# Optimization experiments

Measured on AMD Instinct MI355X. Metric: run time of the kernel, lower is better.

The kernel has to match this reference:

```python
import jax, jax.numpy as jnp
import numpy as np
from jax import lax

NPOINT = 1024
FG_NSAMPLE = 512
TOPK = 2048
NSAMPLE = 32
RADIUS = 0.3
BN_EPS = 1e-5


def masked_fps(xyz, mask, n):
    """Farthest point sampling restricted to points where mask is True.
    xyz: [B,N,3] (grad-stopped), mask: [B,N] bool. Returns int32 [B,n] indices.
    Equivalent to running FPS on the masked subset starting at its first point."""
    xyz = lax.stop_gradient(xyz)

    def one(x, m):
        mind0 = jnp.where(m, jnp.float32(1e10), jnp.float32(-1.0))

        def body(i, carry):
            mind, idxs = carry
            sel = jnp.argmax(mind).astype(jnp.int32)
            d = jnp.sum((x - x[sel]) ** 2, axis=-1)
            mind = jnp.where(m, jnp.minimum(mind, d), jnp.float32(-1.0))
            return mind, idxs.at[i].set(sel)

        _, idxs = lax.fori_loop(0, n, body, (mind0, jnp.zeros((n,), jnp.int32)))
        return idxs

    return jax.vmap(one)(xyz, mask)


def ball_query(xyz, new_xyz, radius, nsample):
    """xyz: [B,N,3], new_xyz: [B,S,3] -> int32 [B,S,nsample] of first neighbors
    within radius (padded with the first found index, as in pointnet2 CUDA)."""
    x = lax.stop_gradient(xyz)
    q = lax.stop_gradient(new_xyz)
    d2 = jnp.sum((q[:, :, None, :] - x[:, None, :, :]) ** 2, axis=-1)  # [B,S,N]
    N = x.shape[1]
    ar = jnp.arange(N, dtype=jnp.float32)
    key = jnp.where(d2 <= radius * radius, ar, jnp.float32(N))
    neg_top, _ = lax.top_k(-key, nsample)  # smallest nsample indices
    idx = (-neg_top).astype(jnp.int32)
    first = idx[..., :1]
    idx = jnp.where(idx >= N, first, idx)
    return jnp.clip(idx, 0, N - 1)


def conv_bn_relu_2d(x, W, g, b):
    # x: [B,C,S,ns], W: [O,C]; 1x1 conv (no bias) + training-mode BN + ReLU
    y = jnp.einsum('oc,bcsn->bosn', W, x)
    mu = y.mean((0, 2, 3), keepdims=True)
    var = y.var((0, 2, 3), keepdims=True)
    y = (y - mu) * lax.rsqrt(var + BN_EPS) * g[None, :, None, None] + b[None, :, None, None]
    return jax.nn.relu(y)


def conv_bn_relu_1d(x, W, g, b):
    # x: [B,C,N]
    y = jnp.einsum('oc,bcn->bon', W, x)
    mu = y.mean((0, 2), keepdims=True)
    var = y.var((0, 2), keepdims=True)
    y = (y - mu) * lax.rsqrt(var + BN_EPS) * g[None, :, None] + b[None, :, None]
    return jax.nn.relu(y)


def batch_gather_points(x, idx):
    # x: [B,N,3], idx: [B,...] -> [B,...,3]
    return jax.vmap(lambda a, i: a[i])(x, idx)


def batch_gather_feats(f, idx):
    # f: [B,C,N], idx: [B,S,ns] -> [B,C,S,ns]
    return jax.vmap(lambda a, i: a[:, i])(f, idx)


def setup_inputs() -> dict:
    key = jax.random.key(0)
    ks = jax.random.split(key, 16)
    B, N, C = 4, 16384, 128
    s = 0.05
    return {
        'xyz': jax.random.uniform(ks[0], (B, N, 3), dtype=jnp.float32),
        'features': jax.random.normal(ks[1], (B, C, N), dtype=jnp.float32),
        # grouped shared MLP: (3+C)->128->128->256
        'w1': jax.random.normal(ks[2], (128, 131), dtype=jnp.float32) * s,
        'g1': jnp.ones((128,), jnp.float32), 'b1': jnp.zeros((128,), jnp.float32),
        'w2': jax.random.normal(ks[3], (128, 128), dtype=jnp.float32) * s,
        'g2': jnp.ones((128,), jnp.float32), 'b2': jnp.zeros((128,), jnp.float32),
        'w3': jax.random.normal(ks[4], (256, 128), dtype=jnp.float32) * s,
        'g3': jnp.ones((256,), jnp.float32), 'b3': jnp.zeros((256,), jnp.float32),
        # fbs mask MLP: C->64->2 (last layer plain conv with bias)
        'fw1': jax.random.normal(ks[5], (64, 128), dtype=jnp.float32) * s,
        'fg1': jnp.ones((64,), jnp.float32), 'fb1': jnp.zeros((64,), jnp.float32),
        'fw2': jax.random.normal(ks[6], (2, 64), dtype=jnp.float32) * s,
        'fbias2': jnp.zeros((2,), jnp.float32),
    }


def reference(xyz, features, w1, g1, b1, w2, g2, b2, w3, g3, b3, fw1, fg1, fb1, fw2, fbias2):
    B, N, _ = xyz.shape
    # --- FBS: foreground/background scoring ---
    h = conv_bn_relu_1d(features, fw1, fg1, fb1)                 # [B,64,N]
    mask_scores = jnp.einsum('oc,bcn->bon', fw2, h) + fbias2[None, :, None]  # [B,2,N]
    soft = jax.nn.softmax(mask_scores, axis=1)
    margin = soft[:, 1, :] - soft[:, 0, :]                        # [B,N]
    _, top_idx = lax.top_k(margin, TOPK)
    fg_mask = jnp.zeros((B, N), bool).at[jnp.arange(B)[:, None], top_idx].set(True)
    # --- mask-restricted FPS on foreground and background ---
    fg_idx = masked_fps(xyz, fg_mask, FG_NSAMPLE)                 # [B,512]
    bg_idx = masked_fps(xyz, ~fg_mask, NPOINT - FG_NSAMPLE)       # [B,512]
    indices = jnp.concatenate([fg_idx, bg_idx], axis=1)          # [B,npoint]
    new_xyz = batch_gather_points(xyz, indices)                   # [B,npoint,3]
    # --- ball query + grouping ---
    idx = ball_query(xyz, new_xyz, RADIUS, NSAMPLE)               # [B,S,ns]
    grouped_xyz = batch_gather_points(xyz, idx)                   # [B,S,ns,3]
    grouped_xyz = grouped_xyz - new_xyz[:, :, None, :]
    grouped_xyz = jnp.transpose(grouped_xyz, (0, 3, 1, 2))        # [B,3,S,ns]
    grouped_feats = batch_gather_feats(features, idx)             # [B,C,S,ns]
    x = jnp.concatenate([grouped_xyz, grouped_feats], axis=1)     # [B,3+C,S,ns]
    # --- shared MLP + max pool over neighbors ---
    x = conv_bn_relu_2d(x, w1, g1, b1)
    x = conv_bn_relu_2d(x, w2, g2, b2)
    x = conv_bn_relu_2d(x, w3, g3, b3)
    new_features = jnp.max(x, axis=-1)                            # [B,256,S]
    return new_xyz, new_features, indices, mask_scores
```

## Files before the change

kernel.cpp:

```cpp
#include <hip/hip_runtime.h>

#define BB 4
#define NPT 16384
#define CIN 128
#define SS 1024
#define NS 32
#define PP 131072
#define TOPKK 2048

typedef unsigned short u16;
typedef unsigned int u32;
typedef unsigned long long u64;
typedef float v2 __attribute__((ext_vector_type(2)));
typedef short bf16x8 __attribute__((ext_vector_type(8)));
typedef float f32x4 __attribute__((ext_vector_type(4)));

__device__ __forceinline__ float bf2f(u32 v){ return __uint_as_float(v << 16); }
__device__ __forceinline__ u16 f2bf(float f){
  u32 u = __float_as_uint(f);
  u32 r = (u + 0x7FFFu + ((u >> 16) & 1u)) >> 16;
  return (u16)r;
}
__device__ __forceinline__ u32 keyOf(float m){
  u32 u = __float_as_uint(m);
  return (u & 0x80000000u) ? ~u : (u | 0x80000000u);
}

__device__ __forceinline__ float row_max16(float v){
  #define STEP(CTRL) { int o_ = __builtin_amdgcn_update_dpp(0, __float_as_int(v), CTRL, 0xf, 0xf, true); \
                       v = fmaxf(v, __int_as_float(o_)); }
  STEP(0x111) STEP(0x112) STEP(0x114) STEP(0x118)
  #undef STEP
  return v;
}

#define OFF_NEWXYZ 0ull
#define OFF_MARGIN 49152ull
#define OFF_FGMASK 311296ull
#define OFF_IDXNB  573440ull
#define OFF_MSTAT  1097728ull
#define OFF_SSA    1098240ull
#define OFF_WT0    1104384ull
#define OFF_W1B    1137152ull
#define OFF_W2B    1178112ull
#define OFF_W3B    1210880ull
#define OFF_MPART  1407488ull
#define OFF_CPART  2456064ull
#define OFF_REGB   10844672ull
#define OFF_REGA   44399104ull
#define WS_NEED    86342144ull

__global__ void k_prep(const float* __restrict__ w1, const float* __restrict__ w2,
                       const float* __restrict__ w3, const float* __restrict__ fw1,
                       float* __restrict__ wt0, u16* __restrict__ w1b, u16* __restrict__ w2b,
                       u16* __restrict__ w3b){
  int gt = blockIdx.x*blockDim.x + threadIdx.x;
  int gs = gridDim.x*blockDim.x;
  for (int i = gt; i < 128*64;  i += gs){ int k=i>>6, m=i&63;  wt0[i] = fw1[m*128+k]; }
  for (int i = gt; i < 128*160; i += gs){ int m=i/160, k=i-m*160; w1b[i] = (k<131)? f2bf(w1[m*131+k]) : (u16)0; }
  for (int i = gt; i < 128*128; i += gs){ w2b[i] = f2bf(w2[i]); }
  for (int i = gt; i < 256*128; i += gs){ w3b[i] = f2bf(w3[i]); }
}

__global__ __launch_bounds__(256) void k_prepT(const float* __restrict__ feat, u16* __restrict__ featT2){
  __shared__ u16 tile[128][66];
  int b = blockIdx.y; int n0 = blockIdx.x * 64;
  int t = threadIdx.x;
  #pragma unroll
  for (int it = 0; it < 32; it++){
    int idx = it*256 + t; int c = idx >> 6, nn = idx & 63;
    tile[c][nn] = f2bf(feat[((size_t)b*CIN + c)*NPT + n0 + nn]);
  }
  __syncthreads();
  for (int it = 0; it < 40; it++){
    int idx = it*256 + t; int nn = idx / 160; int c = idx - nn*160;
    u16 v = (c >= 3 && c < 131) ? tile[c-3][nn] : (u16)0;
    featT2[((size_t)(b*NPT + n0 + nn))*160 + c] = v;
  }
}

__global__ __launch_bounds__(256) void k_gemm_mask(const float* __restrict__ Wt,
                                                   const float* __restrict__ feat,
                                                   float* __restrict__ y0,
                                                   double* __restrict__ mpart){
  __shared__ float As[32][64];
  __shared__ float Bs[32][64];
  int t = threadIdx.x, tx = t & 15, ty = t >> 4;
  int p0 = blockIdx.x * 64; int b = blockIdx.z;
  const float* X = feat + (size_t)b * CIN * NPT;
  float acc[4][4] = {};
  int e = t * 8, ka = e >> 6, ca = e & 63;
  for (int kc = 0; kc < 4; kc++){
    const float* wr = Wt + (size_t)(kc*32 + ka) * 64 + ca;
    float4 w0 = *(const float4*)wr;
    float4 w1v = *(const float4*)(wr + 4);
    const float* br = X + (size_t)(kc*32 + ka) * NPT + p0 + ca;
    float4 b0 = *(const float4*)br;
    float4 b1 = *(const float4*)(br + 4);
    __syncthreads();
    *(float4*)&As[ka][ca] = w0; *(float4*)&As[ka][ca+4] = w1v;
    *(float4*)&Bs[ka][ca] = b0; *(float4*)&Bs[ka][ca+4] = b1;
    __syncthreads();
    #pragma unroll
    for (int k = 0; k < 32; k++){
      float4 a = *(float4*)&As[k][ty*4];
      float4 bq = *(float4*)&Bs[k][tx*4];
      float av[4] = {a.x,a.y,a.z,a.w}; float bw[4] = {bq.x,bq.y,bq.z,bq.w};
      #pragma unroll
      for (int i = 0; i < 4; i++)
        #pragma unroll
        for (int j = 0; j < 4; j++) acc[i][j] = fmaf(av[i], bw[j], acc[i][j]);
    }
  }
  #pragma unroll
  for (int i = 0; i < 4; i++){
    int m = ty*4 + i;
    float4 v = make_float4(acc[i][0], acc[i][1], acc[i][2], acc[i][3]);
    *(float4*)(y0 + ((size_t)(b*64 + m)) * NPT + p0 + tx*4) = v;
  }
  __syncthreads();
  float* red = (float*)As;
  #pragma unroll
  for (int i = 0; i < 4; i++){
    float s = 0.f, q = 0.f;
    #pragma unroll
    for (int j = 0; j < 4; j++){ s += acc[i][j]; q += acc[i][j]*acc[i][j]; }
    red[((ty*4+i)*16 + tx)*2] = s; red[((ty*4+i)*16 + tx)*2 + 1] = q;
  }
  __syncthreads();
  if (t < 64){
    double s = 0.0, q = 0.0;
    for (int x = 0; x < 16; x++){ s += red[(t*16+x)*2]; q += red[(t*16+x)*2+1]; }
    int slot = b*256 + blockIdx.x;
    mpart[((size_t)t*1024 + slot)*2] = s;
    mpart[((size_t)t*1024 + slot)*2 + 1] = q;
  }
}

__global__ void k_mask_stats(const double* __restrict__ mpart, float* __restrict__ mstat){
  int t = threadIdx.x;
  double s = 0.0, q = 0.0;
  for (int i = 0; i < 1024; i++){ s += mpart[((size_t)t*1024 + i)*2]; q += mpart[((size_t)t*1024 + i)*2+1]; }
  double cnt = 65536.0;
  double mu = s/cnt; double var = q/cnt - mu*mu;
  mstat[t*2] = (float)mu; mstat[t*2+1] = 1.0f / sqrtf((float)var + 1e-5f);
}

__global__ __launch_bounds__(256) void k_scores(const float* __restrict__ y0, const float* __restrict__ mstat,
                                                const float* __restrict__ fg1, const float* __restrict__ fb1,
                                                const float* __restrict__ fw2, const float* __restrict__ fbias2,
                                                float* __restrict__ margin, float* __restrict__ out3){
  __shared__ float smu[64], srs[64], sg[64], sb[64], sw[128];
  int t = threadIdx.x; int b = blockIdx.y; int n = blockIdx.x*256 + t;
  if (t < 64){ smu[t] = mstat[t*2]; srs[t] = mstat[t*2+1]; sg[t] = fg1[t]; sb[t] = fb1[t]; }
  if (t < 128) sw[t] = fw2[t];
  __syncthreads();
  float a0 = 0.f, a1 = 0.f;
  const float* yb = y0 + (size_t)b*64*NPT + n;
  for (int o = 0; o < 64; o++){
    float y = yb[(size_t)o * NPT];
    float h = __fmul_rn(__fmul_rn(__fsub_rn(y, smu[o]), srs[o]), sg[o]);
    h = __fadd_rn(h, sb[o]);
    h = fmaxf(h, 0.f);
    a0 = fmaf(sw[o], h, a0);
    a1 = fmaf(sw[64+o], h, a1);
  }
  float s0 = __fadd_rn(a0, fbias2[0]);
  float s1 = __fadd_rn(a1, fbias2[1]);
  out3[(size_t)(b*2)*NPT + n] = s0;
  out3[(size_t)(b*2+1)*NPT + n] = s1;
  float m = fmaxf(s0, s1);
  float e0 = expf(__fsub_rn(s0, m));
  float e1 = expf(__fsub_rn(s1, m));
  float den = __fadd_rn(e0, e1);
  margin[b*NPT + n] = __fsub_rn(__fdiv_rn(e1, den), __fdiv_rn(e0, den));
}

__global__ __launch_bounds__(1024) void k_topk(const float* __restrict__ margin, u32* __restrict__ fgmask){
  int t = threadIdx.x; int b = blockIdx.x;
  int lane = t & 63, wv = t >> 6;
  const float* mg = margin + b*NPT; u32* fm = fgmask + b*NPT;
  __shared__ int hist[256];
  __shared__ int swt[2][16];
  __shared__ u32 s_bin; __shared__ int s_need;
  int need = TOPKK; u32 prefix = 0, kmask = 0;
  for (int r = 0; r < 4; r++){
    int shift = 24 - 8*r;
    if (t < 256) hist[t] = 0;
    __syncthreads();
    for (int j = 0; j < 16; j++){
      u32 key = keyOf(mg[j*1024 + t]);
      if ((key & kmask) == prefix) atomicAdd(&hist[(key >> shift) & 255], 1);
    }
    __syncthreads();
    if (t == 0){
      int cum = 0;
      for (int bin = 255; bin >= 0; bin--){
        int c = hist[bin];
        if (cum + c >= need){ s_bin = (u32)bin; s_need = need - cum; break; }
        cum += c;
      }
    }
    __syncthreads();
    prefix |= s_bin << shift; kmask |= 255u << shift; need = s_need;
    __syncthreads();
  }
  u32 T = prefix;
  int run = 0;
  for (int j = 0; j < 16; j++){
    int n = j*1024 + t;
    u32 key = keyOf(mg[n]);
    int eq = (key == T) ? 1 : 0;
    int gt = (key > T) ? 1 : 0;
    u64 bal = __ballot(eq != 0);
    int lexcl = __popcll(bal & ((1ull << lane) - 1ull));
    if (lane == 0) swt[j & 1][wv] = __popcll(bal);
    __syncthreads();
    int base = 0, tot = 0;
    #pragma unroll
    for (int w = 0; w < 16; w++){
      int c = swt[j & 1][w];
      tot += c;
      if (w < wv) base += c;
    }
    int flag = gt | (eq & ((run + base + lexcl) < need ? 1 : 0));
    fm[n] = (u32)flag;
    run += tot;
  }
}

__global__ __launch_bounds__(1024) void k_compact(const float* __restrict__ xyz, const u32* __restrict__ fgmask,
                                                  float* __restrict__ cx, float* __restrict__ cy,
                                                  float* __restrict__ cz, int* __restrict__ cg){
  int blk = blockIdx.x; int b = blk >> 1; int which = blk & 1;
  const float* xb = xyz + (size_t)b * NPT * 3;
  const u32* mb = fgmask + b*NPT;
  int t = threadIdx.x;
  __shared__ int sc[1024];
  u32 mloc = 0; int cnt = 0;
  int p0 = t*16;
  #pragma unroll
  for (int j = 0; j < 16; j++){
    u32 m = mb[p0+j];
    bool inc = which ? (m == 0u) : (m != 0u);
    mloc |= (inc ? 1u : 0u) << j; cnt += inc ? 1 : 0;
  }
  sc[t] = cnt; __syncthreads();
  for (int off = 1; off < 1024; off <<= 1){
    int v = (t >= off) ? sc[t-off] : 0;
    __syncthreads();
    sc[t] += v;
    __syncthreads();
  }
  int pos = sc[t] - cnt;
  int base = b*16384 + (which ? 2048 : 0);
  for (int j = 0; j < 16; j++){
    if ((mloc >> j) & 1u){
      int p = p0 + j;
      cx[base+pos] = xb[p*3]; cy[base+pos] = xb[p*3+1]; cz[base+pos] = xb[p*3+2];
      cg[base+pos] = p; pos++;
    }
  }
}

template<int NV>
__device__ __forceinline__ void fps_run(const float* __restrict__ cx, const float* __restrict__ cy,
                                        const float* __restrict__ cz, const int* __restrict__ cg,
                                        int b, int which,
                                        float* __restrict__ newxyz, float* __restrict__ out0,
                                        float* __restrict__ out2){
  #pragma clang fp contract(off)
  int t = threadIdx.x;
  __shared__ u64 slots[2][8];
  if (t < 16) ((u64*)slots)[t] = 0ull;
  v2 px[NV], py[NV], pz[NV], mind[NV];
  #pragma unroll
  for (int r = 0; r < NV; r++){
    int p0 = 1024*r + t, p1 = 1024*r + 512 + t;
    px[r].x = cx[p0]; px[r].y = cx[p1];
    py[r].x = cy[p0]; py[r].y = cy[p1];
    pz[r].x = cz[p0]; pz[r].y = cz[p1];
    mind[r].x = 1e10f; mind[r].y = 1e10f;
  }
  __syncthreads();
  float bv = 1e10f; int bi = t;
  for (int it = 0; it < 512; it++){
    u64 key = ((u64)(it+1) << 46) | ((u64)keyOf(bv) << 14) | (u64)(16383 - bi);
    atomicMax((unsigned long long*)&slots[it & 1][t & 7], (unsigned long long)key);
    __syncthreads();
    u64 k0 = slots[it & 1][0];
    #pragma unroll
    for (int i = 1; i < 8; i++){ u64 ki = slots[it & 1][i]; if (ki > k0) k0 = ki; }
    int sel = 16383 - (int)(k0 & 0x3FFFu);
    float xs = cx[sel], ys = cy[sel], zs = cz[sel];
    if (t == 0){
      int s = which*512 + it;
      out2[b*1024 + s] = (float)cg[sel];
      newxyz[(b*1024 + s)*3]   = xs;
      newxyz[(b*1024 + s)*3+1] = ys;
      newxyz[(b*1024 + s)*3+2] = zs;
      out0[(b*1024 + s)*3]   = xs;
      out0[(b*1024 + s)*3+1] = ys;
      out0[(b*1024 + s)*3+2] = zs;
    }
    v2 xs2; xs2.x = xs; xs2.y = xs;
    v2 ys2; ys2.x = ys; ys2.y = ys;
    v2 zs2; zs2.x = zs; zs2.y = zs;
    bv = -1.0f; bi = 16383;
    #pragma unroll
    for (int r = 0; r < NV; r++){
      v2 dx = px[r] - xs2;
      v2 dy = py[r] - ys2;
      v2 dz = pz[r] - zs2;
      v2 qx = dx * dx;
      v2 qy = dy * dy;
      v2 qz = dz * dz;
      v2 s1 = qx + qy;
      v2 d  = s1 + qz;
      float m0 = fminf(mind[r].x, d.x);
      float m1 = fminf(mind[r].y, d.y);
      mind[r].x = m0; mind[r].y = m1;
      if (m0 > bv){ bv = m0; bi = 1024*r + t; }
      if (m1 > bv){ bv = m1; bi = 1024*r + 512 + t; }
    }
  }
}

__global__ __launch_bounds__(512) void k_fps(const float* __restrict__ cx, const float* __restrict__ cy,
                                             const float* __restrict__ cz, const int* __restrict__ cg,
                                             float* __restrict__ newxyz, float* __restrict__ out0,
                                             float* __restrict__ out2){
  int b = blockIdx.x >> 1; int which = blockIdx.x & 1;
  int base = b*16384 + (which ? 2048 : 0);
  if (which) fps_run<14>(cx+base, cy+base, cz+base, cg+base, b, 1, newxyz, out0, out2);
  else       fps_run<2 >(cx+base, cy+base, cz+base, cg+base, b, 0, newxyz, out0, out2);
}

__global__ __launch_bounds__(256) void k_ball(const float* __restrict__ xyz, const float* __restrict__ newxyz,
                                              int* __restrict__ idxnb){
  int t = threadIdx.x; int lane = t & 63;
  int qid = blockIdx.x*4 + (t >> 6);
  int b = qid >> 10;
  const float* xb = xyz + (size_t)b * NPT * 3;
  float qx = newxyz[qid*3], qy = newxyz[qid*3+1], qz = newxyz[qid*3+2];
  int found = 0, first = -1;
  for (int base = 0; base < NPT; base += 64){
    int p = base + lane;
    float x = xb[p*3], y = xb[p*3+1], z = xb[p*3+2];
    float dx = __fsub_rn(qx, x), dy = __fsub_rn(qy, y), dz = __fsub_rn(qz, z);
    float d2 = __fadd_rn(__fadd_rn(__fmul_rn(dx,dx), __fmul_rn(dy,dy)), __fmul_rn(dz,dz));
    bool w = d2 <= 0.09f;
    u64 m = __ballot(w);
    if (first < 0 && m) first = base + __ffsll((unsigned long long)m) - 1;
    if (w){
      int pos = found + __popcll(m & ((1ull << lane) - 1ull));
      if (pos < NS) idxnb[(size_t)qid*NS + pos] = p;
    }
    found += __popcll(m);
    if (found >= NS) break;
  }
  if (first < 0) first = 0;
  if (lane < NS && lane >= found) idxnb[(size_t)qid*NS + lane] = first;
}

__global__ __launch_bounds__(256) void k_buildX(const float* __restrict__ xyz, const float* __restrict__ newxyz,
                                                const int* __restrict__ idxnb, const u16* __restrict__ featT2,
                                                u16* __restrict__ Xb2){
  int pos = blockIdx.x*256 + threadIdx.x;
  int b = pos >> 15; int r = pos & 32767; int s = r >> 5;
  int gi = idxnb[pos] & (NPT - 1);
  const float* xp = xyz + ((size_t)b*NPT + gi) * 3;
  const float* qp = newxyz + ((size_t)(b << 10) + s) * 3;
  u16 d0 = f2bf(__fsub_rn(xp[0], qp[0]));
  u16 d1 = f2bf(__fsub_rn(xp[1], qp[1]));
  u16 d2 = f2bf(__fsub_rn(xp[2], qp[2]));
  const uint4* row = (const uint4*)(featT2 + (size_t)(b*NPT + gi) * 160);
  #pragma unroll
  for (int kg = 0; kg < 20; kg++){
    uint4 u = row[kg];
    if (kg == 0){
      u.x = (u32)d0 | ((u32)d1 << 16);
      u.y = (u.y & 0xFFFF0000u) | (u32)d2;
    }
    *(uint4*)(Xb2 + ((size_t)kg*PP + pos)*8) = u;
  }
}

template<int NKS, int STORE>
__global__ __launch_bounds__(256) void k_mfma(const u16* __restrict__ Wb, int Kpad,
                                              const u16* __restrict__ Xp,
                                              u16* __restrict__ Yp, double* __restrict__ cpart){
  __shared__ float sred[4][16][16][2];
  int t = threadIdx.x;
  int w = t >> 6, lane = t & 63;
  int q = lane >> 4, c = lane & 15;
  int p0 = blockIdx.x * 64, m0 = blockIdx.y * 64;
  int m_w = m0 + w*16;
  f32x4 acc[4] = {{0.f,0.f,0.f,0.f},{0.f,0.f,0.f,0.f},{0.f,0.f,0.f,0.f},{0.f,0.f,0.f,0.f}};
  const u16* arow = Wb + (size_t)(m_w + c) * Kpad + q*8;
  #pragma unroll
  for (int ks = 0; ks < NKS; ks++){
    bf16x8 afrag = *(const bf16x8*)(arow + ks*32);
    #pragma unroll
    for (int pp = 0; pp < 4; pp++){
      int p = p0 + pp*16 + c;
      bf16x8 bfrag = *(const bf16x8*)(Xp + (((size_t)(ks*4 + q) * PP) + p) * 8);
      acc[pp] = __builtin_amdgcn_mfma_f32_16x16x32_bf16(afrag, bfrag, acc[pp], 0, 0, 0);
    }
  }
  #pragma unroll
  for (int reg = 0; reg < 4; reg++){
    float s = 0.f, sq = 0.f;
    #pragma unroll
    for (int pp = 0; pp < 4; pp++){ float v = acc[pp][reg]; s += v; sq += v*v; }
    sred[w][q*4+reg][c][0] = s; sred[w][q*4+reg][c][1] = sq;
  }
  if (STORE){
    int kgm = (m_w + q*4) >> 3;
    int j0 = (m_w + q*4) & 7;
    #pragma unroll
    for (int pp = 0; pp < 4; pp++){
      int p = p0 + pp*16 + c;
      ushort4 pk;
      pk.x = f2bf(acc[pp][0]); pk.y = f2bf(acc[pp][1]); pk.z = f2bf(acc[pp][2]); pk.w = f2bf(acc[pp][3]);
      *(ushort4*)(Yp + (((size_t)kgm * PP) + p) * 8 + j0) = pk;
    }
  }
  __syncthreads();
  if (t < 64){
    int ww = t >> 4, ml = t & 15;
    double s = 0.0, qq = 0.0;
    for (int cc = 0; cc < 16; cc++){ s += sred[ww][ml][cc][0]; qq += sred[ww][ml][cc][1]; }
    cpart[((size_t)(m0 + t) * 2048 + blockIdx.x)*2] = s;
    cpart[((size_t)(m0 + t) * 2048 + blockIdx.x)*2 + 1] = qq;
  }
}

__global__ __launch_bounds__(256) void k_mfma_pool(const u16* __restrict__ Wb,
                                                   const u16* __restrict__ Xp,
                                                   const float2* __restrict__ ss2,
                                                   float* __restrict__ out1){
  int t = threadIdx.x;
  int w = t >> 6, lane = t & 63;
  int q = lane >> 4, c = lane & 15;
  int p0 = blockIdx.x * 64, m0 = blockIdx.y * 64;
  int m_w = m0 + w*16;
  f32x4 acc[4] = {{0.f,0.f,0.f,0.f},{0.f,0.f,0.f,0.f},{0.f,0.f,0.f,0.f},{0.f,0.f,0.f,0.f}};
  const u16* arow = Wb + (size_t)(m_w + c) * 128 + q*8;
  #pragma unroll
  for (int ks = 0; ks < 4; ks++){
    bf16x8 afrag = *(const bf16x8*)(arow + ks*32);
    #pragma unroll
    for (int pp = 0; pp < 4; pp++){
      int p = p0 + pp*16 + c;
      bf16x8 bfrag = *(const bf16x8*)(Xp + (((size_t)(ks*4 + q) * PP) + p) * 8);
      acc[pp] = __builtin_amdgcn_mfma_f32_16x16x32_bf16(afrag, bfrag, acc[pp], 0, 0, 0);
    }
  }
  int qid0 = blockIdx.x*2;
  #pragma unroll
  for (int reg = 0; reg < 4; reg++){
    int m = m_w + q*4 + reg;
    float2 af = ss2[m];
    float x0 = fmaxf(0.f, fmaf(acc[0][reg], af.x, af.y));
    float x1 = fmaxf(0.f, fmaf(acc[1][reg], af.x, af.y));
    float x2 = fmaxf(0.f, fmaf(acc[2][reg], af.x, af.y));
    float x3 = fmaxf(0.f, fmaf(acc[3][reg], af.x, af.y));
    float v0 = row_max16(fmaxf(x0, x1));
    float v1 = row_max16(fmaxf(x2, x3));
    if (c == 15){
      int qa = qid0, qb = qid0 + 1;
      out1[((size_t)(qa >> 10) << 18) + (size_t)m*1024 + (qa & 1023)] = v0;
      out1[((size_t)(qb >> 10) << 18) + (size_t)m*1024 + (qb & 1023)] = v1;
    }
  }
}

__global__ __launch_bounds__(256) void k_stats_conv(const double* __restrict__ cpart,
                                                    const float* __restrict__ g, const float* __restrict__ bt,
                                                    float2* __restrict__ ssv){
  __shared__ double rs_[256], rq_[256];
  int ch = blockIdx.x, t = threadIdx.x;
  double s = 0.0, q = 0.0;
  for (int i = t; i < 2048; i += 256){ s += cpart[((size_t)ch*2048 + i)*2]; q += cpart[((size_t)ch*2048 + i)*2+1]; }
  rs_[t] = s; rq_[t] = q; __syncthreads();
  for (int off = 128; off; off >>= 1){
    if (t < off){ rs_[t] += rs_[t+off]; rq_[t] += rq_[t+off]; }
    __syncthreads();
  }
  if (t == 0){
    double cnt = (double)PP;
    double mu = rs_[0]/cnt; double var = rq_[0]/cnt - mu*mu;
    float rsf = 1.0f / sqrtf((float)var + 1e-5f);
    double rsd = (double)rsf;
    double gd = (double)g[ch]; double bd = (double)bt[ch];
    ssv[ch] = make_float2((float)(rsd*gd), (float)(bd - mu*rsd*gd));
  }
}

__global__ __launch_bounds__(256) void k_affine(u16* __restrict__ y, const float2* __restrict__ aff){
  int tid = blockIdx.x*256 + threadIdx.x;
  int kg = tid >> 17; int p = tid & (PP - 1);
  uint4* ptr = (uint4*)(y + (((size_t)kg*PP) + p)*8);
  uint4 u = *ptr;
  u32 us[4] = {u.x, u.y, u.z, u.w};
  u32 outp[4];
  #pragma unroll
  for (int i = 0; i < 4; i++){
    float2 a0 = aff[kg*8 + 2*i], a1 = aff[kg*8 + 2*i + 1];
    float v0 = fmaxf(0.f, fmaf(bf2f(us[i] & 0xFFFFu), a0.x, a0.y));
    float v1 = fmaxf(0.f, fmaf(bf2f(us[i] >> 16),     a1.x, a1.y));
    outp[i] = (u32)f2bf(v0) | ((u32)f2bf(v1) << 16);
  }
  *ptr = make_uint4(outp[0], outp[1], outp[2], outp[3]);
}

extern "C" void kernel_launch(void* const* d_in, const int* in_sizes, int n_in,
                              void* d_out, int out_size, void* d_ws, size_t ws_size,
                              hipStream_t stream){
  (void)in_sizes; (void)n_in; (void)out_size;
  if (ws_size < WS_NEED) return;
  const float* xyz    = (const float*)d_in[0];
  const float* feat   = (const float*)d_in[1];
  const float* w1     = (const float*)d_in[2];
  const float* g1     = (const float*)d_in[3];
  const float* b1     = (const float*)d_in[4];
  const float* w2     = (const float*)d_in[5];
  const float* g2     = (const float*)d_in[6];
  const float* b2     = (const float*)d_in[7];
  const float* w3     = (const float*)d_in[8];
  const float* g3     = (const float*)d_in[9];
  const float* b3     = (const float*)d_in[10];
  const float* fw1    = (const float*)d_in[11];
  const float* fg1    = (const float*)d_in[12];
  const float* fb1    = (const float*)d_in[13];
  const float* fw2    = (const float*)d_in[14];
  const float* fbias2 = (const float*)d_in[15];

  char* ws = (char*)d_ws;
  float*  newxyz = (float*)(ws + OFF_NEWXYZ);
  float*  margin = (float*)(ws + OFF_MARGIN);
  u32*    fgmask = (u32*)(ws + OFF_FGMASK);
  int*    idxnb  = (int*)(ws + OFF_IDXNB);
  float*  mstat  = (float*)(ws + OFF_MSTAT);
  float2* ss0    = (float2*)(ws + OFF_SSA);
  float2* ss1    = ss0 + 128;
  float2* ss2    = ss0 + 256;
  float*  wt0    = (float*)(ws + OFF_WT0);
  u16*    w1b    = (u16*)(ws + OFF_W1B);
  u16*    w2b    = (u16*)(ws + OFF_W2B);
  u16*    w3b    = (u16*)(ws + OFF_W3B);
  double* mpart  = (double*)(ws + OFF_MPART);
  double* cpart  = (double*)(ws + OFF_CPART);
  u16*    featT2 = (u16*)(ws + OFF_REGB);
  u16*    Y1p    = (u16*)(ws + OFF_REGB);
  float*  y0     = (float*)(ws + OFF_REGA);
  float*  cx     = (float*)(ws + OFF_REGA);
  float*  cy     = cx + 4*16384;
  float*  cz     = cy + 4*16384;
  int*    cg     = (int*)(cz + 4*16384);
  u16*    Xb2    = (u16*)(ws + OFF_REGA);
  u16*    Y2p    = (u16*)(ws + OFF_REGA);

  float* out  = (float*)d_out;
  float* out0 = out;
  float* out1 = out + 12288;
  float* out2 = out + 1060864;
  float* out3 = out + 1064960;

  k_prep<<<dim3(256), dim3(256), 0, stream>>>(w1, w2, w3, fw1, wt0, w1b, w2b, w3b);
  k_prepT<<<dim3(256,4), dim3(256), 0, stream>>>(feat, featT2);
  k_gemm_mask<<<dim3(256,1,4), dim3(256), 0, stream>>>(wt0, feat, y0, mpart);
  k_mask_stats<<<dim3(1), dim3(64), 0, stream>>>(mpart, mstat);
  k_scores<<<dim3(64,4), dim3(256), 0, stream>>>(y0, mstat, fg1, fb1, fw2, fbias2, margin, out3);
  k_topk<<<dim3(4), dim3(1024), 0, stream>>>(margin, fgmask);
  k_compact<<<dim3(8), dim3(1024), 0, stream>>>(xyz, fgmask, cx, cy, cz, cg);
  k_fps<<<dim3(8), dim3(512), 0, stream>>>(cx, cy, cz, cg, newxyz, out0, out2);
  k_ball<<<dim3(1024), dim3(256), 0, stream>>>(xyz, newxyz, idxnb);
  k_buildX<<<dim3(512), dim3(256), 0, stream>>>(xyz, newxyz, idxnb, featT2, Xb2);
  k_mfma<5,1><<<dim3(2048,2), dim3(256), 0, stream>>>(w1b, 160, Xb2, Y1p, cpart);
  k_stats_conv<<<dim3(128), dim3(256), 0, stream>>>(cpart, g1, b1, ss0);
  k_affine<<<dim3(8192), dim3(256), 0, stream>>>(Y1p, ss0);
  k_mfma<4,1><<<dim3(2048,2), dim3(256), 0, stream>>>(w2b, 128, Y1p, Y2p, cpart);
  k_stats_conv<<<dim3(128), dim3(256), 0, stream>>>(cpart, g2, b2, ss1);
  k_affine<<<dim3(8192), dim3(256), 0, stream>>>(Y2p, ss1);
  k_mfma<4,0><<<dim3(2048,4), dim3(256), 0, stream>>>(w3b, 128, Y2p, (u16*)nullptr, cpart);
  k_stats_conv<<<dim3(256), dim3(256), 0, stream>>>(cpart, g3, b3, ss2);
  k_mfma_pool<<<dim3(2048,4), dim3(256), 0, stream>>>(w3b, Y2p, ss2, out1);
}
```

Baseline: 1.169 ms.

## Fuse BN affine+ReLU into MFMA B-operand load and cover all output channels per block

Removes the standalone k_affine passes by applying the previous layer's BN scale/shift and ReLU to the bf16 B fragments as they are loaded inside the MFMA kernels. Each block now computes every output-channel tile (MT tiles) for its 64 points, so the activation tile is read once instead of once per y-block. The mask partial-sum layout is also transposed so k_mask_stats threads read coalesced. In exchange, the affine math is redone for each consumer read, the third layer's affine is applied twice (stats pass and pool pass), and per-thread accumulator registers grow, which may reduce occupancy.

```diff
diff --git a/kernel.cpp b/kernel.cpp
--- a/kernel.cpp
+++ b/kernel.cpp
@@ -132,15 +132,15 @@
     double s = 0.0, q = 0.0;
     for (int x = 0; x < 16; x++){ s += red[(t*16+x)*2]; q += red[(t*16+x)*2+1]; }
     int slot = b*256 + blockIdx.x;
-    mpart[((size_t)t*1024 + slot)*2] = s;
-    mpart[((size_t)t*1024 + slot)*2 + 1] = q;
+    mpart[((size_t)slot*64 + t)*2] = s;
+    mpart[((size_t)slot*64 + t)*2 + 1] = q;
   }
 }
 
 __global__ void k_mask_stats(const double* __restrict__ mpart, float* __restrict__ mstat){
   int t = threadIdx.x;
   double s = 0.0, q = 0.0;
-  for (int i = 0; i < 1024; i++){ s += mpart[((size_t)t*1024 + i)*2]; q += mpart[((size_t)t*1024 + i)*2+1]; }
+  for (int i = 0; i < 1024; i++){ s += mpart[((size_t)i*64 + t)*2]; q += mpart[((size_t)i*64 + t)*2+1]; }
   double cnt = 65536.0;
   double mu = s/cnt; double var = q/cnt - mu*mu;
   mstat[t*2] = (float)mu; mstat[t*2+1] = 1.0f / sqrtf((float)var + 1e-5f);
@@ -386,92 +386,148 @@
   }
 }
 
-template<int NKS, int STORE>
+template<int NKS, int MT, int AFF, int STORE>
 __global__ __launch_bounds__(256) void k_mfma(const u16* __restrict__ Wb, int Kpad,
-                                              const u16* __restrict__ Xp,
+                                              const u16* __restrict__ Xp, const float2* __restrict__ aff,
                                               u16* __restrict__ Yp, double* __restrict__ cpart){
-  __shared__ float sred[4][16][16][2];
+  __shared__ float sred[MT][4][16][16][2];
   int t = threadIdx.x;
   int w = t >> 6, lane = t & 63;
   int q = lane >> 4, c = lane & 15;
-  int p0 = blockIdx.x * 64, m0 = blockIdx.y * 64;
-  int m_w = m0 + w*16;
-  f32x4 acc[4] = {{0.f,0.f,0.f,0.f},{0.f,0.f,0.f,0.f},{0.f,0.f,0.f,0.f},{0.f,0.f,0.f,0.f}};
-  const u16* arow = Wb + (size_t)(m_w + c) * Kpad + q*8;
+  int p0 = blockIdx.x * 64;
+  f32x4 acc[MT][4];
+  #pragma unroll
+  for (int mt = 0; mt < MT; mt++)
+    #pragma unroll
+    for (int pp = 0; pp < 4; pp++) acc[mt][pp] = (f32x4){0.f,0.f,0.f,0.f};
   #pragma unroll
   for (int ks = 0; ks < NKS; ks++){
-    bf16x8 afrag = *(const bf16x8*)(arow + ks*32);
+    float2 af[8];
+    if (AFF){
+      #pragma unroll
+      for (int j = 0; j < 8; j++) af[j] = aff[(ks*4 + q)*8 + j];
+    }
+    bf16x8 afrag[MT];
+    #pragma unroll
+    for (int mt = 0; mt < MT; mt++){
+      int m_w = (mt*4 + w)*16;
+      afrag[mt] = *(const bf16x8*)(Wb + (size_t)(m_w + c)*Kpad + ks*32 + q*8);
+    }
     #pragma unroll
     for (int pp = 0; pp < 4; pp++){
       int p = p0 + pp*16 + c;
       bf16x8 bfrag = *(const bf16x8*)(Xp + (((size_t)(ks*4 + q) * PP) + p) * 8);
-      acc[pp] = __builtin_amdgcn_mfma_f32_16x16x32_bf16(afrag, bfrag, acc[pp], 0, 0, 0);
-    }
-  }
-  #pragma unroll
-  for (int reg = 0; reg < 4; reg++){
-    float s = 0.f, sq = 0.f;
-    #pragma unroll
-    for (int pp = 0; pp < 4; pp++){ float v = acc[pp][reg]; s += v; sq += v*v; }
-    sred[w][q*4+reg][c][0] = s; sred[w][q*4+reg][c][1] = sq;
-  }
-  if (STORE){
-    int kgm = (m_w + q*4) >> 3;
-    int j0 = (m_w + q*4) & 7;
-    #pragma unroll
-    for (int pp = 0; pp < 4; pp++){
-      int p = p0 + pp*16 + c;
-      ushort4 pk;
-      pk.x = f2bf(acc[pp][0]); pk.y = f2bf(acc[pp][1]); pk.z = f2bf(acc[pp][2]); pk.w = f2bf(acc[pp][3]);
-      *(ushort4*)(Yp + (((size_t)kgm * PP) + p) * 8 + j0) = pk;
+      if (AFF){
+        u32* bu = (u32*)&bfrag;
+        #pragma unroll
+        for (int i = 0; i < 4; i++){
+          float v0 = fmaxf(0.f, fmaf(bf2f(bu[i] & 0xFFFFu), af[2*i].x,   af[2*i].y));
+          float v1 = fmaxf(0.f, fmaf(bf2f(bu[i] >> 16),     af[2*i+1].x, af[2*i+1].y));
+          bu[i] = (u32)f2bf(v0) | ((u32)f2bf(v1) << 16);
+        }
+      }
+      #pragma unroll
+      for (int mt = 0; mt < MT; mt++)
+        acc[mt][pp] = __builtin_amdgcn_mfma_f32_16x16x32_bf16(afrag[mt], bfrag, acc[mt][pp], 0, 0, 0);
+    }
+  }
+  #pragma unroll
+  for (int mt = 0; mt < MT; mt++){
+    #pragma unroll
+    for (int reg = 0; reg < 4; reg++){
+      float s = 0.f, sq = 0.f;
+      #pragma unroll
+      for (int pp = 0; pp < 4; pp++){ float v = acc[mt][pp][reg]; s += v; sq += v*v; }
+      sred[mt][w][q*4+reg][c][0] = s; sred[mt][w][q*4+reg][c][1] = sq;
+    }
+    if (STORE){
+      int m_w = (mt*4 + w)*16;
+      int kgm = (m_w + q*4) >> 3;
+      int j0 = (m_w + q*4) & 7;
+      #pragma unroll
+      for (int pp = 0; pp < 4; pp++){
+        int p = p0 + pp*16 + c;
+        ushort4 pk;
+        pk.x = f2bf(acc[mt][pp][0]); pk.y = f2bf(acc[mt][pp][1]);
+        pk.z = f2bf(acc[mt][pp][2]); pk.w = f2bf(acc[mt][pp][3]);
+        *(ushort4*)(Yp + (((size_t)kgm * PP) + p) * 8 + j0) = pk;
+      }
     }
   }
   __syncthreads();
   if (t < 64){
     int ww = t >> 4, ml = t & 15;
-    double s = 0.0, qq = 0.0;
-    for (int cc = 0; cc < 16; cc++){ s += sred[ww][ml][cc][0]; qq += sred[ww][ml][cc][1]; }
-    cpart[((size_t)(m0 + t) * 2048 + blockIdx.x)*2] = s;
-    cpart[((size_t)(m0 + t) * 2048 + blockIdx.x)*2 + 1] = qq;
+    #pragma unroll
+    for (int mt = 0; mt < MT; mt++){
+      double s = 0.0, qq = 0.0;
+      for (int cc = 0; cc < 16; cc++){ s += sred[mt][ww][ml][cc][0]; qq += sred[mt][ww][ml][cc][1]; }
+      int ch = (mt*4 + ww)*16 + ml;
+      cpart[((size_t)ch * 2048 + blockIdx.x)*2] = s;
+      cpart[((size_t)ch * 2048 + blockIdx.x)*2 + 1] = qq;
+    }
   }
 }
 
 __global__ __launch_bounds__(256) void k_mfma_pool(const u16* __restrict__ Wb,
                                                    const u16* __restrict__ Xp,
+                                                   const float2* __restrict__ aff1,
                                                    const float2* __restrict__ ss2,
                                                    float* __restrict__ out1){
   int t = threadIdx.x;
   int w = t >> 6, lane = t & 63;
   int q = lane >> 4, c = lane & 15;
-  int p0 = blockIdx.x * 64, m0 = blockIdx.y * 64;
-  int m_w = m0 + w*16;
-  f32x4 acc[4] = {{0.f,0.f,0.f,0.f},{0.f,0.f,0.f,0.f},{0.f,0.f,0.f,0.f},{0.f,0.f,0.f,0.f}};
-  const u16* arow = Wb + (size_t)(m_w + c) * 128 + q*8;
+  int p0 = blockIdx.x * 64;
+  f32x4 acc[4][4];
+  #pragma unroll
+  for (int mt = 0; mt < 4; mt++)
+    #pragma unroll
+    for (int pp = 0; pp < 4; pp++) acc[mt][pp] = (f32x4){0.f,0.f,0.f,0.f};
   #pragma unroll
   for (int ks = 0; ks < 4; ks++){
-    bf16x8 afrag = *(const bf16x8*)(arow + ks*32);
+    float2 af[8];
+    #pragma unroll
+    for (int j = 0; j < 8; j++) af[j] = aff1[(ks*4 + q)*8 + j];
+    bf16x8 afrag[4];
+    #pragma unroll
+    for (int mt = 0; mt < 4; mt++){
+      int m_w = (mt*4 + w)*16;
+      afrag[mt] = *(const bf16x8*)(Wb + (size_t)(m_w + c)*128 + ks*32 + q*8);
+    }
     #pragma unroll
     for (int pp = 0; pp < 4; pp++){
       int p = p0 + pp*16 + c;
       bf16x8 bfrag = *(const bf16x8*)(Xp + (((size_t)(ks*4 + q) * PP) + p) * 8);
-      acc[pp] = __builtin_amdgcn_mfma_f32_16x16x32_bf16(afrag, bfrag, acc[pp], 0, 0, 0);
+      u32* bu = (u32*)&bfrag;
+      #pragma unroll
+      for (int i = 0; i < 4; i++){
+        float v0 = fmaxf(0.f, fmaf(bf2f(bu[i] & 0xFFFFu), af[2*i].x,   af[2*i].y));
+        float v1 = fmaxf(0.f, fmaf(bf2f(bu[i] >> 16),     af[2*i+1].x, af[2*i+1].y));
+        bu[i] = (u32)f2bf(v0) | ((u32)f2bf(v1) << 16);
+      }
+      #pragma unroll
+      for (int mt = 0; mt < 4; mt++)
+        acc[mt][pp] = __builtin_amdgcn_mfma_f32_16x16x32_bf16(afrag[mt], bfrag, acc[mt][pp], 0, 0, 0);
     }
   }
   int qid0 = blockIdx.x*2;
   #pragma unroll
-  for (int reg = 0; reg < 4; reg++){
-    int m = m_w + q*4 + reg;
-    float2 af = ss2[m];
-    float x0 = fmaxf(0.f, fmaf(acc[0][reg], af.x, af.y));
-    float x1 = fmaxf(0.f, fmaf(acc[1][reg], af.x, af.y));
-    float x2 = fmaxf(0.f, fmaf(acc[2][reg], af.x, af.y));
-    float x3 = fmaxf(0.f, fmaf(acc[3][reg], af.x, af.y));
-    float v0 = row_max16(fmaxf(x0, x1));
-    float v1 = row_max16(fmaxf(x2, x3));
-    if (c == 15){
-      int qa = qid0, qb = qid0 + 1;
-      out1[((size_t)(qa >> 10) << 18) + (size_t)m*1024 + (qa & 1023)] = v0;
-      out1[((size_t)(qb >> 10) << 18) + (size_t)m*1024 + (qb & 1023)] = v1;
+  for (int mt = 0; mt < 4; mt++){
+    int m_w = (mt*4 + w)*16;
+    #pragma unroll
+    for (int reg = 0; reg < 4; reg++){
+      int m = m_w + q*4 + reg;
+      float2 af = ss2[m];
+      float x0 = fmaxf(0.f, fmaf(acc[mt][0][reg], af.x, af.y));
+      float x1 = fmaxf(0.f, fmaf(acc[mt][1][reg], af.x, af.y));
+      float x2 = fmaxf(0.f, fmaf(acc[mt][2][reg], af.x, af.y));
+      float x3 = fmaxf(0.f, fmaf(acc[mt][3][reg], af.x, af.y));
+      float v0 = row_max16(fmaxf(x0, x1));
+      float v1 = row_max16(fmaxf(x2, x3));
+      if (c == 15){
+        int qa = qid0, qb = qid0 + 1;
+        out1[((size_t)(qa >> 10) << 18) + (size_t)m*1024 + (qa & 1023)] = v0;
+        out1[((size_t)(qb >> 10) << 18) + (size_t)m*1024 + (qb & 1023)] = v1;
+      }
     }
   }
 }
@@ -496,23 +552,6 @@
     double gd = (double)g[ch]; double bd = (double)bt[ch];
     ssv[ch] = make_float2((float)(rsd*gd), (float)(bd - mu*rsd*gd));
   }
-}
-
-__global__ __launch_bounds__(256) void k_affine(u16* __restrict__ y, const float2* __restrict__ aff){
-  int tid = blockIdx.x*256 + threadIdx.x;
-  int kg = tid >> 17; int p = tid & (PP - 1);
-  uint4* ptr = (uint4*)(y + (((size_t)kg*PP) + p)*8);
-  uint4 u = *ptr;
-  u32 us[4] = {u.x, u.y, u.z, u.w};
-  u32 outp[4];
-  #pragma unroll
-  for (int i = 0; i < 4; i++){
-    float2 a0 = aff[kg*8 + 2*i], a1 = aff[kg*8 + 2*i + 1];
-    float v0 = fmaxf(0.f, fmaf(bf2f(us[i] & 0xFFFFu), a0.x, a0.y));
-    float v1 = fmaxf(0.f, fmaf(bf2f(us[i] >> 16),     a1.x, a1.y));
-    outp[i] = (u32)f2bf(v0) | ((u32)f2bf(v1) << 16);
-  }
-  *ptr = make_uint4(outp[0], outp[1], outp[2], outp[3]);
 }
 
 extern "C" void kernel_launch(void* const* d_in, const int* in_sizes, int n_in,
@@ -578,13 +617,11 @@
   k_fps<<<dim3(8), dim3(512), 0, stream>>>(cx, cy, cz, cg, newxyz, out0, out2);
   k_ball<<<dim3(1024), dim3(256), 0, stream>>>(xyz, newxyz, idxnb);
   k_buildX<<<dim3(512), dim3(256), 0, stream>>>(xyz, newxyz, idxnb, featT2, Xb2);
-  k_mfma<5,1><<<dim3(2048,2), dim3(256), 0, stream>>>(w1b, 160, Xb2, Y1p, cpart);
+  k_mfma<5,2,0,1><<<dim3(2048), dim3(256), 0, stream>>>(w1b, 160, Xb2, nullptr, Y1p, cpart);
   k_stats_conv<<<dim3(128), dim3(256), 0, stream>>>(cpart, g1, b1, ss0);
-  k_affine<<<dim3(8192), dim3(256), 0, stream>>>(Y1p, ss0);
-  k_mfma<4,1><<<dim3(2048,2), dim3(256), 0, stream>>>(w2b, 128, Y1p, Y2p, cpart);
+  k_mfma<4,2,1,1><<<dim3(2048), dim3(256), 0, stream>>>(w2b, 128, Y1p, ss0, Y2p, cpart);
   k_stats_conv<<<dim3(128), dim3(256), 0, stream>>>(cpart, g2, b2, ss1);
-  k_affine<<<dim3(8192), dim3(256), 0, stream>>>(Y2p, ss1);
-  k_mfma<4,0><<<dim3(2048,4), dim3(256), 0, stream>>>(w3b, 128, Y2p, (u16*)nullptr, cpart);
+  k_mfma<4,4,1,0><<<dim3(2048), dim3(256), 0, stream>>>(w3b, 128, Y2p, ss1, (u16*)nullptr, cpart);
   k_stats_conv<<<dim3(256), dim3(256), 0, stream>>>(cpart, g3, b3, ss2);
-  k_mfma_pool<<<dim3(2048,4), dim3(256), 0, stream>>>(w3b, Y2p, ss2, out1);
-}
+  k_mfma_pool<<<dim3(2048), dim3(256), 0, stream>>>(w3b, Y2p, ss1, ss2, out1);
+}
```

Measured after the change: 1.145 ms. 2.0% less time.
